# Kernel tuning notes

Measured on AMD Instinct MI355X. Metric: run time of the kernel, lower is better.

The kernel has to match this reference:

```python
import jax, jax.numpy as jnp
import numpy as np

TYPE_NUM = 4
CHILDS = [2, 2, 2, 2]
NODE_NUM = 8          # sum(CHILDS)
HEADS = 4
GROUP = 4
IN, MID, OUT = 256, 256, 256


def _mask():
    m = np.zeros((TYPE_NUM, NODE_NUM), np.float32)
    s = 0
    for i, c in enumerate(CHILDS):
        m[i, s:s + c] = 1.0
        s += c
    return jnp.asarray(m)


def _graph_feature(x, node_num):
    # x: [B, L, C] -> [B, M, node_num+1, C] with M = (L-1)//node_num
    B, L, C = x.shape
    node_x = x[:, 1:, :].reshape(B, -1, C * node_num)
    M = node_x.shape[1]
    src = x[:, :M, :]
    return jnp.concatenate([node_x, src], axis=2).reshape(B, M, node_num + 1, C)


def _conv1d(x, w, b, groups):
    # x: [N, C, T], w: [O, C//groups, K], stride == K, 'VALID' -> length-1 output
    y = jax.lax.conv_general_dilated(
        x, w, window_strides=(w.shape[-1],), padding='VALID',
        feature_group_count=groups, dimension_numbers=('NCH', 'OIH', 'NCH'))
    return y + b[None, :, None]


def _agg(feat, attn, mask):
    # feat: [B, M, node_num+1, C]; attn: [B, M, node_num, HEADS] (softmaxed)
    B, M, A, C = feat.shape
    n = A - 1
    nf = feat[:, :, :-1, :].reshape(B, M, n, HEADS, C // HEADS) * attn[..., None]
    nf = nf.reshape(B, M, n, C)
    agg = jnp.einsum('tn,bmnc->bmtc', mask, nf)  # masked group-sum (bmm with block mask)
    return agg, feat[:, :, -1, :]


def setup_inputs() -> dict:
    key = jax.random.key(0)
    ks = jax.random.split(key, 12)
    B, L = 4, 32777

    def lin(k, fi, fo):
        return jax.random.normal(k, (fi, fo), jnp.float32) / np.sqrt(fi).astype(np.float32)

    def convw(k, o, i, kk):
        return jax.random.normal(k, (o, i, kk), jnp.float32) / np.sqrt(i * kk).astype(np.float32)

    return {
        'input': jax.random.normal(ks[0], (B, L, IN), jnp.float32),
        'gt': jax.random.normal(ks[1], (B, 512, IN), jnp.float32),
        'w_att': lin(ks[2], IN, HEADS), 'b_att': jnp.zeros((HEADS,), jnp.float32),
        'w_gt1': lin(ks[3], IN, MID), 'b_gt1': jnp.zeros((MID,), jnp.float32),
        'w_gt2': lin(ks[4], MID, OUT), 'b_gt2': jnp.zeros((OUT,), jnp.float32),
        'w_agg1': convw(ks[5], MID, IN // GROUP, TYPE_NUM), 'b_agg1': jnp.zeros((MID,), jnp.float32),
        'w_src1': convw(ks[6], MID, IN // GROUP, 1), 'b_src1': jnp.zeros((MID,), jnp.float32),
        'w_agg2': convw(ks[7], OUT, MID // GROUP, TYPE_NUM), 'b_agg2': jnp.zeros((OUT,), jnp.float32),
        'w_src2': convw(ks[8], OUT, MID // GROUP, 1), 'b_src2': jnp.zeros((OUT,), jnp.float32),
    }


def reference(input, gt, w_att, b_att, w_gt1, b_gt1, w_gt2, b_gt2,
              w_agg1, b_agg1, w_src1, b_src1, w_agg2, b_agg2, w_src2, b_src2):
    mask = _mask()
    B = gt.shape[0]
    # gt branch (eval mode: dropout = identity)
    gt1 = jax.nn.relu(gt @ w_gt1 + b_gt1)   # [B, 512, MID]
    gt2 = jax.nn.relu(gt1 @ w_gt2 + b_gt2)  # [B, 512, OUT]

    # ---- layer 1 ----
    feat = _graph_feature(input, NODE_NUM)   # [B, M, 9, IN]
    M = feat.shape[1]
    ft = feat[:, :, -1:, :] + feat[:, :, :-1, :]          # source + each neighbor
    attn = jax.nn.softmax(ft @ w_att + b_att, axis=2)     # softmax over node dim
    node, src = _agg(feat, attn, mask)                    # [B,M,T,IN], [B,M,IN]
    BM = B * M
    node = jnp.transpose(node.reshape(BM, TYPE_NUM, IN), (0, 2, 1))  # [BM, IN, T]
    src = src.reshape(BM, IN, 1)
    node1 = jax.nn.relu(_conv1d(node, w_agg1, b_agg1, GROUP))[:, :, 0]  # [BM, MID]
    src1 = jax.nn.relu(_conv1d(src, w_src1, b_src1, GROUP))[:, :, 0]

    nf1 = node1.reshape(B, M, MID)[:, 0, :]
    d1 = gt1[:, 0, :] - nf1
    score1 = 1.0 - jnp.exp(-0.5 * jnp.sum(d1 * d1, axis=1))  # [B]

    out1 = (node1 + src1).reshape(B, M, MID)

    # ---- layer 2 (reuses attn truncated to M2) ----
    feat2 = _graph_feature(out1, NODE_NUM)  # [B, M2, 9, MID]
    M2 = feat2.shape[1]
    node2, src2 = _agg(feat2, attn[:, :M2], mask)
    BM2 = B * M2
    node2 = jnp.transpose(node2.reshape(BM2, TYPE_NUM, MID), (0, 2, 1))
    src2 = src2.reshape(BM2, MID, 1)
    node2c = jax.nn.relu(_conv1d(node2, w_agg2, b_agg2, GROUP))  # [BM2, OUT, 1]

    nf2 = node2c.reshape(B, M2, OUT)
    d2 = (gt2[:, :M2, :] - nf2).reshape(-1, OUT)
    score2 = 1.0 - jnp.exp(-0.5 * jnp.sum(d2 * d2, axis=1))  # [B*M2]

    src2c = jax.nn.relu(_conv1d(src2, w_src2, b_src2, GROUP))
    output = (node2c + src2c).reshape(-1, OUT)  # [B*M2, OUT]
    return output, score1, score2
```

## Files before the change

### kernel.cpp

```cpp
#include <hip/hip_runtime.h>

typedef unsigned short u16;
typedef unsigned int   u32;
typedef __attribute__((ext_vector_type(8))) short short8;
typedef __attribute__((ext_vector_type(4))) float f32x4;

#define BB  4
#define LL  32777
#define MM  4097
#define MMP 4112
#define MM2 512

__device__ __forceinline__ float b2f(u16 u) { return __uint_as_float(((u32)u) << 16); }
__device__ __forceinline__ u16 f2bf(float f) {
    u32 u = __float_as_uint(f);
    return (u16)((u + 0x7fffu + ((u >> 16) & 1u)) >> 16);
}
__device__ __forceinline__ u32 pk(float a, float b) {
    return (u32)f2bf(a) | ((u32)f2bf(b) << 16);
}
__device__ __forceinline__ float bflo(u32 u) { return __uint_as_float(u << 16); }
__device__ __forceinline__ float bfhi(u32 u) { return __uint_as_float(u & 0xffff0000u); }

__global__ __launch_bounds__(256) void prep_w(const float* __restrict__ wagg1,
                                              const float* __restrict__ wagg2,
                                              const float* __restrict__ wsrc1,
                                              const float* __restrict__ wsrc2,
                                              const float* __restrict__ watt,
                                              u16* __restrict__ wA1, u16* __restrict__ wA2,
                                              u16* __restrict__ wS1, u16* __restrict__ wS2,
                                              u16* __restrict__ wattB) {
    int idx = blockIdx.x * 256 + threadIdx.x;
    if (idx < 131072) {
        int which = idx >> 16;
        int e = idx & 65535;
        int j = e & 7, lane = (e >> 3) & 63, mt = (e >> 9) & 3, kc = (e >> 11) & 7, g = (e >> 14) & 3;
        int ol = mt * 16 + (lane & 15);
        int k = kc * 32 + (lane >> 4) * 8 + j;
        int t = k >> 6, ci = k & 63;
        const float* src = which ? wagg2 : wagg1;
        u16* dst = which ? wA2 : wA1;
        dst[e] = f2bf(src[(g * 64 + ol) * 256 + ci * 4 + t]);
    } else if (idx < 163840) {
        int e2 = idx - 131072;
        int which = e2 >> 14;
        int e = e2 & 16383;
        int j = e & 7, lane = (e >> 3) & 63, mt = (e >> 9) & 3, kc = (e >> 11) & 1, g = (e >> 12) & 3;
        int ol = mt * 16 + (lane & 15);
        int k = kc * 32 + (lane >> 4) * 8 + j;
        const float* src = which ? wsrc2 : wsrc1;
        u16* dst = which ? wS2 : wS1;
        dst[e] = f2bf(src[(g * 64 + ol) * 64 + k]);
    } else if (idx < 167936) {
        int e = idx - 163840;
        int j = e & 7, lane = (e >> 3) & 63, kc = e >> 9;
        int h = lane & 15, quad = lane >> 4;
        int k = kc * 32 + quad * 8 + j;
        wattB[e] = (h < 4) ? f2bf(watt[k * 4 + h]) : (u16)0;
    }
}

__global__ __launch_bounds__(256) void gemm2_fused_k(
    const float* __restrict__ gt, const float* __restrict__ W1, const float* __restrict__ b1,
    const float* __restrict__ W2, const float* __restrict__ b2,
    float* __restrict__ gt2, float* __restrict__ gt1m0) {
    __shared__ float sh[256][8];
    int tid = threadIdx.x;
    int row0 = blockIdx.x * 8;
    {
        int r = tid >> 5, j = tid & 31;
        const float4* a4 = (const float4*)(gt + (size_t)(row0 + r) * 256 + j * 8);
        float4 v0 = a4[0], v1 = a4[1];
        sh[j * 8 + 0][r] = v0.x; sh[j * 8 + 1][r] = v0.y;
        sh[j * 8 + 2][r] = v0.z; sh[j * 8 + 3][r] = v0.w;
        sh[j * 8 + 4][r] = v1.x; sh[j * 8 + 5][r] = v1.y;
        sh[j * 8 + 6][r] = v1.z; sh[j * 8 + 7][r] = v1.w;
    }
    __syncthreads();
    int o = tid;
    float acc[8];
    {
        float bo = b1[o];
        #pragma unroll
        for (int i = 0; i < 8; ++i) acc[i] = bo;
    }
    #pragma unroll 4
    for (int k = 0; k < 256; ++k) {
        float wv = W1[k * 256 + o];
        const float4* ap = (const float4*)&sh[k][0];
        float4 a0 = ap[0], a1 = ap[1];
        acc[0] = fmaf(a0.x, wv, acc[0]); acc[1] = fmaf(a0.y, wv, acc[1]);
        acc[2] = fmaf(a0.z, wv, acc[2]); acc[3] = fmaf(a0.w, wv, acc[3]);
        acc[4] = fmaf(a1.x, wv, acc[4]); acc[5] = fmaf(a1.y, wv, acc[5]);
        acc[6] = fmaf(a1.z, wv, acc[6]); acc[7] = fmaf(a1.w, wv, acc[7]);
    }
    #pragma unroll
    for (int i = 0; i < 8; ++i) acc[i] = fmaxf(acc[i], 0.f);
    if ((row0 & 511) == 0) gt1m0[(row0 >> 9) * 256 + o] = acc[0];
    __syncthreads();
    #pragma unroll
    for (int i = 0; i < 8; ++i) sh[o][i] = acc[i];
    __syncthreads();
    {
        float bo = b2[o];
        #pragma unroll
        for (int i = 0; i < 8; ++i) acc[i] = bo;
    }
    #pragma unroll 4
    for (int k = 0; k < 256; ++k) {
        float wv = W2[k * 256 + o];
        const float4* ap = (const float4*)&sh[k][0];
        float4 a0 = ap[0], a1 = ap[1];
        acc[0] = fmaf(a0.x, wv, acc[0]); acc[1] = fmaf(a0.y, wv, acc[1]);
        acc[2] = fmaf(a0.z, wv, acc[2]); acc[3] = fmaf(a0.w, wv, acc[3]);
        acc[4] = fmaf(a1.x, wv, acc[4]); acc[5] = fmaf(a1.y, wv, acc[5]);
        acc[6] = fmaf(a1.z, wv, acc[6]); acc[7] = fmaf(a1.w, wv, acc[7]);
    }
    #pragma unroll
    for (int i = 0; i < 8; ++i) gt2[(size_t)(row0 + i) * 256 + o] = fmaxf(acc[i], 0.f);
}

__global__ __launch_bounds__(256, 2) void l1fused_k(
    const float* __restrict__ x, const float* __restrict__ batt,
    const u16* __restrict__ wA1, const u16* __restrict__ wS1,
    const u16* __restrict__ wattB,
    const float* __restrict__ bagg1, const float* __restrict__ bsrc1,
    float* __restrict__ attnf, u16* __restrict__ out1, float* __restrict__ n1m0) {
    __shared__ u16   sh_node[128 * 256];
    __shared__ u16   sh_srcq[16 * 256];
    __shared__ float shR[1088];

    int tid = threadIdx.x;
    int lane = tid & 63, w = tid >> 6;
    int quad = lane >> 4;
    int b = blockIdx.y;
    int p0 = blockIdx.x * 16;

    {
        int cseg = lane & 15;
        int rsub = lane >> 4;
        const float* xb = x + (size_t)b * LL * 256;
        #pragma unroll
        for (int i = 0; i < 9; ++i) {
            int r = (w * 9 + i) * 4 + rsub;
            int grow, key; u16* dst;
            if (r < 128) {
                int pos = r >> 3, nn = r & 7;
                int gp = p0 + pos; int gpc = gp < MM ? gp : MM - 1;
                grow = 1 + 8 * gpc + nn;
                dst = sh_node + r * 256;
                key = ((r >> 3) ^ r) & 7;
            } else {
                int q = r - 128;
                int gp = p0 + q; int gpc = gp < MM ? gp : MM - 1;
                grow = gpc;
                dst = sh_srcq + q * 256;
                key = q & 7;
            }
            const float4* src4 = (const float4*)(xb + (size_t)grow * 256 + cseg * 16);
            float4 v0 = src4[0], v1 = src4[1], v2 = src4[2], v3 = src4[3];
            uint4 o0, o1;
            o0.x = pk(v0.x, v0.y); o0.y = pk(v0.z, v0.w);
            o0.z = pk(v1.x, v1.y); o0.w = pk(v1.z, v1.w);
            o1.x = pk(v2.x, v2.y); o1.y = pk(v2.z, v2.w);
            o1.z = pk(v3.x, v3.y); o1.w = pk(v3.z, v3.w);
            int cb0 = cseg * 2;
            *(uint4*)(dst + ((cb0 ^ key) * 8))       = o0;
            *(uint4*)(dst + (((cb0 + 1) ^ key) * 8)) = o1;
        }
    }
    __syncthreads();

    {
        short8 wB[8];
        #pragma unroll
        for (int kc = 0; kc < 8; ++kc) wB[kc] = *(const short8*)(wattB + kc * 512 + lane * 8);
        int m = lane & 15;
        int h = lane & 15;
        #pragma unroll
        for (int ti = 0; ti < 2; ++ti) {
            int mt = w * 2 + ti;
            int r = mt * 16 + m;
            int key = ((r >> 3) ^ r) & 7;
            const u16* rowp = sh_node + r * 256;
            f32x4 acc = (f32x4){0.f, 0.f, 0.f, 0.f};
            #pragma unroll
            for (int kc = 0; kc < 8; ++kc) {
                int cb = kc * 4 + quad;
                short8 aF = *(const short8*)(rowp + ((cb ^ key) * 8));
                acc = __builtin_amdgcn_mfma_f32_16x16x32_bf16(aF, wB[kc], acc, 0, 0, 0);
            }
            if (h < 4) {
                #pragma unroll
                for (int r2 = 0; r2 < 4; ++r2)
                    shR[(mt * 16 + quad * 4 + r2) * 4 + h] = acc[r2];
            }
        }
        if (w == 3) {
            int key = m & 7;
            const u16* rowp = sh_srcq + m * 256;
            f32x4 acc = (f32x4){0.f, 0.f, 0.f, 0.f};
            #pragma unroll
            for (int kc = 0; kc < 8; ++kc) {
                int cb = kc * 4 + quad;
                short8 aF = *(const short8*)(rowp + ((cb ^ key) * 8));
                acc = __builtin_amdgcn_mfma_f32_16x16x32_bf16(aF, wB[kc], acc, 0, 0, 0);
            }
            if (h < 4) {
                #pragma unroll
                for (int r2 = 0; r2 < 4; ++r2)
                    shR[512 + (quad * 4 + r2) * 4 + h] = acc[r2];
            }
        }
    }
    __syncthreads();

    if (tid < 64) {
        int q = tid >> 2, h = tid & 3;
        float base = shR[512 + q * 4 + h] + batt[h];
        float l[8], mx = -3.0e38f;
        #pragma unroll
        for (int n = 0; n < 8; ++n) { l[n] = shR[(q * 8 + n) * 4 + h] + base; mx = fmaxf(mx, l[n]); }
        float s = 0.f;
        #pragma unroll
        for (int n = 0; n < 8; ++n) { l[n] = __expf(l[n] - mx); s += l[n]; }
        float inv = 1.f / s;
        int gp = p0 + q;
        float* at = shR + 576;
        #pragma unroll
        for (int n = 0; n < 8; ++n) {
            float aa = l[n] * inv;
            at[(n * 4 + h) * 16 + q] = aa;
            if (gp < MM2) attnf[(((size_t)b * MM2 + gp) * 8 + n) * 4 + h] = aa;
        }
    }
    __syncthreads();

    int g = w;
    int col = lane & 15;
    float aT[8];
    {
        const float* at = shR + 576;
        #pragma unroll
        for (int nn = 0; nn < 8; ++nn) aT[nn] = at[(nn * 4 + g) * 16 + col];
    }
    f32x4 accn[4], accs[4];
    #pragma unroll
    for (int mt = 0; mt < 4; ++mt) { accn[mt] = (f32x4){0,0,0,0}; accs[mt] = (f32x4){0,0,0,0}; }

    #pragma unroll
    for (int kc = 0; kc < 8; ++kc) {
        int k0 = kc * 32 + quad * 8;
        int t = k0 >> 6, ci0 = k0 & 63;
        int cb = (g * 64 + ci0) >> 3;
        int r0 = col * 8 + 2 * t;
        int key0 = (col ^ (2 * t)) & 7, key1 = (col ^ (2 * t + 1)) & 7;
        short8 n0 = *(const short8*)(sh_node + r0 * 256 + ((cb ^ key0) * 8));
        short8 n1 = *(const short8*)(sh_node + (r0 + 1) * 256 + ((cb ^ key1) * 8));
        float a0 = aT[2 * t], a1 = aT[2 * t + 1];
        union { uint4 u; short8 s; } cv;
        #pragma unroll
        for (int e = 0; e < 4; ++e) {
            float lo = fmaf(a0, b2f((u16)n0[2 * e]),     a1 * b2f((u16)n1[2 * e]));
            float hi = fmaf(a0, b2f((u16)n0[2 * e + 1]), a1 * b2f((u16)n1[2 * e + 1]));
            ((u32*)&cv.u)[e] = pk(lo, hi);
        }
        short8 bB = cv.s;
        #pragma unroll
        for (int mt = 0; mt < 4; ++mt) {
            short8 aA = *(const short8*)(wA1 + (((g * 8 + kc) * 4 + mt) * 512 + lane * 8));
            accn[mt] = __builtin_amdgcn_mfma_f32_16x16x32_bf16(aA, bB, accn[mt], 0, 0, 0);
        }
    }
    #pragma unroll
    for (int kc = 0; kc < 2; ++kc) {
        int cb = (g * 64 + kc * 32 + quad * 8) >> 3;
        short8 bS = *(const short8*)(sh_srcq + col * 256 + ((cb ^ (col & 7)) * 8));
        #pragma unroll
        for (int mt = 0; mt < 4; ++mt) {
            short8 aS = *(const short8*)(wS1 + (((g * 2 + kc) * 4 + mt) * 512 + lane * 8));
            accs[mt] = __builtin_amdgcn_mfma_f32_16x16x32_bf16(aS, bS, accs[mt], 0, 0, 0);
        }
    }
    __syncthreads();

    u16* outt = sh_srcq;
    #pragma unroll
    for (int mt = 0; mt < 4; ++mt) {
        int ob = g * 64 + mt * 16 + quad * 4;
        float v[4], n1v[4];
        #pragma unroll
        for (int r = 0; r < 4; ++r) {
            int o = ob + r;
            float n1 = fmaxf(accn[mt][r] + bagg1[o], 0.f);
            float s1 = fmaxf(accs[mt][r] + bsrc1[o], 0.f);
            n1v[r] = n1;
            v[r] = n1 + s1;
        }
        u32* wp = (u32*)&outt[col * 256 + ob];
        wp[0] = pk(v[0], v[1]);
        wp[1] = pk(v[2], v[3]);
        if (blockIdx.x == 0 && col == 0) {
            #pragma unroll
            for (int r = 0; r < 4; ++r) n1m0[b * 256 + ob + r] = n1v[r];
        }
    }
    __syncthreads();
    for (int j = tid; j < 512; j += 256) {
        int pos = j >> 5, cc = (j & 31) * 8;
        if (p0 + pos < MM)
            *(uint4*)&out1[((size_t)b * MMP + p0 + pos) * 256 + cc] = *(const uint4*)&outt[pos * 256 + cc];
    }
}

__global__ __launch_bounds__(256) void score1_k(const float* __restrict__ gt1m0,
                                                const float* __restrict__ n1m0,
                                                float* __restrict__ score1p) {
    int b = blockIdx.x, tid = threadIdx.x;
    __shared__ float red[4];
    float d = gt1m0[b * 256 + tid] - n1m0[b * 256 + tid];
    float v = d * d;
    #pragma unroll
    for (int off = 32; off > 0; off >>= 1) v += __shfl_down(v, off, 64);
    if ((tid & 63) == 0) red[tid >> 6] = v;
    __syncthreads();
    if (tid == 0) score1p[b] = 1.f - __expf(-0.5f * (red[0] + red[1] + red[2] + red[3]));
}

__global__ __launch_bounds__(256) void l2conv_k(
    const u16* __restrict__ out1, const float* __restrict__ attnf,
    const float* __restrict__ gt2,
    const u16* __restrict__ wA2, const u16* __restrict__ wS2,
    const float* __restrict__ bagg2, const float* __restrict__ bsrc2,
    float* __restrict__ outp, float* __restrict__ score2p) {
    __shared__ char shraw[16 * 268 * 4 * 2];
    __shared__ float shred[128];

    int tid = threadIdx.x;
    int b = blockIdx.y;
    int p0 = blockIdx.x * 8;
    u16* aggl = (u16*)shraw;

    {
        int pos16 = tid >> 4, cc = tid & 15;
        int pos = pos16 < 8 ? pos16 : 7;
        int m = p0 + pos;
        int c0 = cc * 16;
        int h = c0 >> 6;
        const float* arow = attnf + ((size_t)b * MM2 + m) * 32;
        #pragma unroll
        for (int t = 0; t < 4; ++t) {
            float a0 = arow[(2 * t) * 4 + h];
            float a1 = arow[(2 * t + 1) * 4 + h];
            const uint4* r0 = (const uint4*)(out1 + ((size_t)b * MMP + 1 + 8 * m + 2 * t) * 256 + c0);
            const uint4* r1 = (const uint4*)(out1 + ((size_t)b * MMP + 2 + 8 * m + 2 * t) * 256 + c0);
            u32 w[8];
            #pragma unroll
            for (int v = 0; v < 2; ++v) {
                uint4 p = r0[v], q = r1[v];
                u32 pv[4] = {p.x, p.y, p.z, p.w};
                u32 qv[4] = {q.x, q.y, q.z, q.w};
                #pragma unroll
                for (int e = 0; e < 4; ++e) {
                    float lo = fmaf(bflo(pv[e]), a0, bflo(qv[e]) * a1);
                    float hi = fmaf(bfhi(pv[e]), a0, bfhi(qv[e]) * a1);
                    w[v * 4 + e] = pk(lo, hi);
                }
            }
            u32* dst = (u32*)&aggl[pos16 * 1024 + h * 256 + t * 64 + (c0 & 63)];
            ((uint4*)dst)[0] = make_uint4(w[0], w[1], w[2], w[3]);
            ((uint4*)dst)[1] = make_uint4(w[4], w[5], w[6], w[7]);
        }
    }
    __syncthreads();

    int lane = tid & 63, g = tid >> 6;
    int col = lane & 15, quad = lane >> 4;
    f32x4 accn[4], accs[4];
    #pragma unroll
    for (int mt = 0; mt < 4; ++mt) { accn[mt] = (f32x4){0,0,0,0}; accs[mt] = (f32x4){0,0,0,0}; }

    #pragma unroll
    for (int kc = 0; kc < 8; ++kc) {
        short8 bB = *(const short8*)&aggl[col * 1024 + g * 256 + kc * 32 + quad * 8];
        #pragma unroll
        for (int mt = 0; mt < 4; ++mt) {
            short8 aA = *(const short8*)(wA2 + (((g * 8 + kc) * 4 + mt) * 512 + lane * 8));
            accn[mt] = __builtin_amdgcn_mfma_f32_16x16x32_bf16(aA, bB, accn[mt], 0, 0, 0);
        }
    }
    {
        int pcol = col < 8 ? col : 7;
        #pragma unroll
        for (int kc = 0; kc < 2; ++kc) {
            short8 bS = *(const short8*)(out1 + ((size_t)b * MMP + p0 + pcol) * 256 + g * 64 + kc * 32 + quad * 8);
            #pragma unroll
            for (int mt = 0; mt < 4; ++mt) {
                short8 aS = *(const short8*)(wS2 + (((g * 2 + kc) * 4 + mt) * 512 + lane * 8));
                accs[mt] = __builtin_amdgcn_mfma_f32_16x16x32_bf16(aS, bS, accs[mt], 0, 0, 0);
            }
        }
    }
    __syncthreads();

    float* outt = (float*)shraw;
    float* n2t  = outt + 16 * 268;
    #pragma unroll
    for (int mt = 0; mt < 4; ++mt) {
        #pragma unroll
        for (int r = 0; r < 4; ++r) {
            int o = g * 64 + mt * 16 + quad * 4 + r;
            float n2 = fmaxf(accn[mt][r] + bagg2[o], 0.f);
            float s2 = fmaxf(accs[mt][r] + bsrc2[o], 0.f);
            outt[col * 268 + o] = n2 + s2;
            n2t[col * 268 + o] = n2;
        }
    }
    __syncthreads();

    for (int j = tid; j < 512; j += 256) {
        int pos = j >> 6, cc = (j & 63) * 4;
        *(float4*)&outp[((size_t)b * MM2 + p0 + pos) * 256 + cc] = *(const float4*)&outt[pos * 268 + cc];
    }
    if (tid < 128) {
        int pos = tid >> 4, kk = tid & 15;
        const float* grow = gt2 + ((size_t)b * MM2 + p0 + pos) * 256 + kk * 16;
        const float* nrow = n2t + pos * 268 + kk * 16;
        float s = 0.f;
        #pragma unroll
        for (int c = 0; c < 16; ++c) { float d = grow[c] - nrow[c]; s = fmaf(d, d, s); }
        shred[pos * 16 + kk] = s;
    }
    __syncthreads();
    if (tid < 8) {
        float s = 0.f;
        #pragma unroll
        for (int kk = 0; kk < 16; ++kk) s += shred[tid * 16 + kk];
        score2p[(size_t)b * MM2 + p0 + tid] = 1.f - __expf(-0.5f * s);
    }
}

extern "C" void kernel_launch(void* const* d_in, const int* in_sizes, int n_in,
                              void* d_out, int out_size, void* d_ws, size_t ws_size,
                              hipStream_t stream) {
    const float* x     = (const float*)d_in[0];
    const float* gt    = (const float*)d_in[1];
    const float* watt  = (const float*)d_in[2];
    const float* batt  = (const float*)d_in[3];
    const float* wgt1  = (const float*)d_in[4];
    const float* bgt1  = (const float*)d_in[5];
    const float* wgt2  = (const float*)d_in[6];
    const float* bgt2  = (const float*)d_in[7];
    const float* wagg1 = (const float*)d_in[8];
    const float* bagg1 = (const float*)d_in[9];
    const float* wsrc1 = (const float*)d_in[10];
    const float* bsrc1 = (const float*)d_in[11];
    const float* wagg2 = (const float*)d_in[12];
    const float* bagg2 = (const float*)d_in[13];
    const float* wsrc2 = (const float*)d_in[14];
    const float* bsrc2 = (const float*)d_in[15];

    char* ws = (char*)d_ws;
    float* ws_gt2  = (float*)(ws + 0);
    float* attnf   = (float*)(ws + 2097152);
    float* n1m0    = (float*)(ws + 2359296);
    float* gt1m0   = (float*)(ws + 2363392);
    u16*   wA1     = (u16*)(ws + 2367488);
    u16*   wS1     = (u16*)(ws + 2498560);
    u16*   wA2     = (u16*)(ws + 2531328);
    u16*   wS2     = (u16*)(ws + 2662400);
    u16*   wattB   = (u16*)(ws + 2695168);
    u16*   out1    = (u16*)(ws + 2703360);

    float* outp    = (float*)d_out;
    float* score1p = outp + 524288;
    float* score2p = outp + 524292;

    prep_w<<<dim3(656), dim3(256), 0, stream>>>(wagg1, wagg2, wsrc1, wsrc2, watt,
                                                wA1, wA2, wS1, wS2, wattB);
    gemm2_fused_k<<<dim3(256), dim3(256), 0, stream>>>(gt, wgt1, bgt1, wgt2, bgt2, ws_gt2, gt1m0);
    l1fused_k<<<dim3(257, 4), dim3(256), 0, stream>>>(x, batt, wA1, wS1, wattB, bagg1, bsrc1,
                                                      attnf, out1, n1m0);
    score1_k<<<dim3(4), dim3(256), 0, stream>>>(gt1m0, n1m0, score1p);
    l2conv_k<<<dim3(64, 4), dim3(256), 0, stream>>>(out1, attnf, ws_gt2, wA2, wS2, bagg2, bsrc2,
                                                    outp, score2p);
}
```

Baseline: 307.1 us.

## Halve l1fused tile to raise occupancy and merge small kernels into neighbors

The layer-1 fused kernel now handles 8 positions per block instead of 16. That halves its shared memory, raises the launch-bounds occupancy target from 2 to 4, and doubles the grid. The weight-prep and gt GEMM kernels are merged into one launch, and the score1 reduction becomes an extra block column of the layer-2 kernel, cutting the launch count from five to three. The price is half-filled MFMA tiles in the source path (only 8 of 16 columns are useful) and more redundant weight loads per block.

```diff
diff --git a/kernel.cpp b/kernel.cpp
--- a/kernel.cpp
+++ b/kernel.cpp
@@ -22,51 +22,49 @@
 __device__ __forceinline__ float bflo(u32 u) { return __uint_as_float(u << 16); }
 __device__ __forceinline__ float bfhi(u32 u) { return __uint_as_float(u & 0xffff0000u); }
 
-__global__ __launch_bounds__(256) void prep_w(const float* __restrict__ wagg1,
-                                              const float* __restrict__ wagg2,
-                                              const float* __restrict__ wsrc1,
-                                              const float* __restrict__ wsrc2,
-                                              const float* __restrict__ watt,
-                                              u16* __restrict__ wA1, u16* __restrict__ wA2,
-                                              u16* __restrict__ wS1, u16* __restrict__ wS2,
-                                              u16* __restrict__ wattB) {
-    int idx = blockIdx.x * 256 + threadIdx.x;
-    if (idx < 131072) {
-        int which = idx >> 16;
-        int e = idx & 65535;
-        int j = e & 7, lane = (e >> 3) & 63, mt = (e >> 9) & 3, kc = (e >> 11) & 7, g = (e >> 14) & 3;
-        int ol = mt * 16 + (lane & 15);
-        int k = kc * 32 + (lane >> 4) * 8 + j;
-        int t = k >> 6, ci = k & 63;
-        const float* src = which ? wagg2 : wagg1;
-        u16* dst = which ? wA2 : wA1;
-        dst[e] = f2bf(src[(g * 64 + ol) * 256 + ci * 4 + t]);
-    } else if (idx < 163840) {
-        int e2 = idx - 131072;
-        int which = e2 >> 14;
-        int e = e2 & 16383;
-        int j = e & 7, lane = (e >> 3) & 63, mt = (e >> 9) & 3, kc = (e >> 11) & 1, g = (e >> 12) & 3;
-        int ol = mt * 16 + (lane & 15);
-        int k = kc * 32 + (lane >> 4) * 8 + j;
-        const float* src = which ? wsrc2 : wsrc1;
-        u16* dst = which ? wS2 : wS1;
-        dst[e] = f2bf(src[(g * 64 + ol) * 64 + k]);
-    } else if (idx < 167936) {
-        int e = idx - 163840;
-        int j = e & 7, lane = (e >> 3) & 63, kc = e >> 9;
-        int h = lane & 15, quad = lane >> 4;
-        int k = kc * 32 + quad * 8 + j;
-        wattB[e] = (h < 4) ? f2bf(watt[k * 4 + h]) : (u16)0;
-    }
-}
-
-__global__ __launch_bounds__(256) void gemm2_fused_k(
+__global__ __launch_bounds__(256) void setup_k(
+    const float* __restrict__ wagg1, const float* __restrict__ wagg2,
+    const float* __restrict__ wsrc1, const float* __restrict__ wsrc2,
+    const float* __restrict__ watt,
+    u16* __restrict__ wA1, u16* __restrict__ wA2,
+    u16* __restrict__ wS1, u16* __restrict__ wS2, u16* __restrict__ wattB,
     const float* __restrict__ gt, const float* __restrict__ W1, const float* __restrict__ b1,
     const float* __restrict__ W2, const float* __restrict__ b2,
     float* __restrict__ gt2, float* __restrict__ gt1m0) {
     __shared__ float sh[256][8];
     int tid = threadIdx.x;
-    int row0 = blockIdx.x * 8;
+    if (blockIdx.x < 656) {
+        int idx = blockIdx.x * 256 + tid;
+        if (idx < 131072) {
+            int which = idx >> 16;
+            int e = idx & 65535;
+            int j = e & 7, lane = (e >> 3) & 63, mt = (e >> 9) & 3, kc = (e >> 11) & 7, g = (e >> 14) & 3;
+            int ol = mt * 16 + (lane & 15);
+            int k = kc * 32 + (lane >> 4) * 8 + j;
+            int t = k >> 6, ci = k & 63;
+            const float* src = which ? wagg2 : wagg1;
+            u16* dst = which ? wA2 : wA1;
+            dst[e] = f2bf(src[(g * 64 + ol) * 256 + ci * 4 + t]);
+        } else if (idx < 163840) {
+            int e2 = idx - 131072;
+            int which = e2 >> 14;
+            int e = e2 & 16383;
+            int j = e & 7, lane = (e >> 3) & 63, mt = (e >> 9) & 3, kc = (e >> 11) & 1, g = (e >> 12) & 3;
+            int ol = mt * 16 + (lane & 15);
+            int k = kc * 32 + (lane >> 4) * 8 + j;
+            const float* src = which ? wsrc2 : wsrc1;
+            u16* dst = which ? wS2 : wS1;
+            dst[e] = f2bf(src[(g * 64 + ol) * 64 + k]);
+        } else {
+            int e = idx - 163840;
+            int j = e & 7, lane = (e >> 3) & 63, kc = e >> 9;
+            int h = lane & 15, quad = lane >> 4;
+            int k = kc * 32 + quad * 8 + j;
+            wattB[e] = (h < 4) ? f2bf(watt[k * 4 + h]) : (u16)0;
+        }
+        return;
+    }
+    int row0 = (blockIdx.x - 656) * 8;
     {
         int r = tid >> 5, j = tid & 31;
         const float4* a4 = (const float4*)(gt + (size_t)(row0 + r) * 256 + j * 8);
@@ -120,53 +118,54 @@
     for (int i = 0; i < 8; ++i) gt2[(size_t)(row0 + i) * 256 + o] = fmaxf(acc[i], 0.f);
 }
 
-__global__ __launch_bounds__(256, 2) void l1fused_k(
+__global__ __launch_bounds__(256, 4) void l1fused_k(
     const float* __restrict__ x, const float* __restrict__ batt,
     const u16* __restrict__ wA1, const u16* __restrict__ wS1,
     const u16* __restrict__ wattB,
     const float* __restrict__ bagg1, const float* __restrict__ bsrc1,
     float* __restrict__ attnf, u16* __restrict__ out1, float* __restrict__ n1m0) {
-    __shared__ u16   sh_node[128 * 256];
-    __shared__ u16   sh_srcq[16 * 256];
-    __shared__ float shR[1088];
+    __shared__ u16   sh_node[64 * 256];
+    __shared__ u16   sh_srcq[8 * 256];
+    __shared__ float shR[576];
 
     int tid = threadIdx.x;
     int lane = tid & 63, w = tid >> 6;
     int quad = lane >> 4;
     int b = blockIdx.y;
-    int p0 = blockIdx.x * 16;
-
-    {
-        int cseg = lane & 15;
-        int rsub = lane >> 4;
+    int p0 = blockIdx.x * 8;
+
+    {
+        int rslot = tid >> 4, cseg = tid & 15;
         const float* xb = x + (size_t)b * LL * 256;
         #pragma unroll
-        for (int i = 0; i < 9; ++i) {
-            int r = (w * 9 + i) * 4 + rsub;
-            int grow, key; u16* dst;
-            if (r < 128) {
-                int pos = r >> 3, nn = r & 7;
-                int gp = p0 + pos; int gpc = gp < MM ? gp : MM - 1;
-                grow = 1 + 8 * gpc + nn;
-                dst = sh_node + r * 256;
-                key = ((r >> 3) ^ r) & 7;
-            } else {
-                int q = r - 128;
-                int gp = p0 + q; int gpc = gp < MM ? gp : MM - 1;
-                grow = gpc;
-                dst = sh_srcq + q * 256;
-                key = q & 7;
-            }
-            const float4* src4 = (const float4*)(xb + (size_t)grow * 256 + cseg * 16);
-            float4 v0 = src4[0], v1 = src4[1], v2 = src4[2], v3 = src4[3];
-            uint4 o0, o1;
-            o0.x = pk(v0.x, v0.y); o0.y = pk(v0.z, v0.w);
-            o0.z = pk(v1.x, v1.y); o0.w = pk(v1.z, v1.w);
-            o1.x = pk(v2.x, v2.y); o1.y = pk(v2.z, v2.w);
-            o1.z = pk(v3.x, v3.y); o1.w = pk(v3.z, v3.w);
-            int cb0 = cseg * 2;
-            *(uint4*)(dst + ((cb0 ^ key) * 8))       = o0;
-            *(uint4*)(dst + (((cb0 + 1) ^ key) * 8)) = o1;
+        for (int pass = 0; pass < 5; ++pass) {
+            int r = pass * 16 + rslot;
+            if (r < 72) {
+                int grow, key; u16* dst;
+                if (r < 64) {
+                    int pos = r >> 3, nn = r & 7;
+                    int gp = p0 + pos; int gpc = gp < MM ? gp : MM - 1;
+                    grow = 1 + 8 * gpc + nn;
+                    dst = sh_node + r * 256;
+                    key = (pos ^ nn) & 7;
+                } else {
+                    int q = r - 64;
+                    int gp = p0 + q; int gpc = gp < MM ? gp : MM - 1;
+                    grow = gpc;
+                    dst = sh_srcq + q * 256;
+                    key = q & 7;
+                }
+                const float4* src4 = (const float4*)(xb + (size_t)grow * 256 + cseg * 16);
+                float4 v0 = src4[0], v1 = src4[1], v2 = src4[2], v3 = src4[3];
+                uint4 o0, o1;
+                o0.x = pk(v0.x, v0.y); o0.y = pk(v0.z, v0.w);
+                o0.z = pk(v1.x, v1.y); o0.w = pk(v1.z, v1.w);
+                o1.x = pk(v2.x, v2.y); o1.y = pk(v2.z, v2.w);
+                o1.z = pk(v3.x, v3.y); o1.w = pk(v3.z, v3.w);
+                int cb0 = cseg * 2;
+                *(uint4*)(dst + ((cb0 ^ key) * 8))       = o0;
+                *(uint4*)(dst + (((cb0 + 1) ^ key) * 8)) = o1;
+            }
         }
     }
     __syncthreads();
@@ -177,11 +176,9 @@
         for (int kc = 0; kc < 8; ++kc) wB[kc] = *(const short8*)(wattB + kc * 512 + lane * 8);
         int m = lane & 15;
         int h = lane & 15;
-        #pragma unroll
-        for (int ti = 0; ti < 2; ++ti) {
-            int mt = w * 2 + ti;
-            int r = mt * 16 + m;
-            int key = ((r >> 3) ^ r) & 7;
+        {
+            int r = w * 16 + m;
+            int key = ((r >> 3) ^ (r & 7)) & 7;
             const u16* rowp = sh_node + r * 256;
             f32x4 acc = (f32x4){0.f, 0.f, 0.f, 0.f};
             #pragma unroll
@@ -193,12 +190,13 @@
             if (h < 4) {
                 #pragma unroll
                 for (int r2 = 0; r2 < 4; ++r2)
-                    shR[(mt * 16 + quad * 4 + r2) * 4 + h] = acc[r2];
+                    shR[(w * 16 + quad * 4 + r2) * 4 + h] = acc[r2];
             }
         }
         if (w == 3) {
-            int key = m & 7;
-            const u16* rowp = sh_srcq + m * 256;
+            int ms = m < 8 ? m : 7;
+            int key = ms & 7;
+            const u16* rowp = sh_srcq + ms * 256;
             f32x4 acc = (f32x4){0.f, 0.f, 0.f, 0.f};
             #pragma unroll
             for (int kc = 0; kc < 8; ++kc) {
@@ -208,16 +206,18 @@
             }
             if (h < 4) {
                 #pragma unroll
-                for (int r2 = 0; r2 < 4; ++r2)
-                    shR[512 + (quad * 4 + r2) * 4 + h] = acc[r2];
-            }
-        }
-    }
-    __syncthreads();
-
-    if (tid < 64) {
+                for (int r2 = 0; r2 < 4; ++r2) {
+                    int rr = quad * 4 + r2;
+                    if (rr < 8) shR[256 + rr * 4 + h] = acc[r2];
+                }
+            }
+        }
+    }
+    __syncthreads();
+
+    if (tid < 32) {
         int q = tid >> 2, h = tid & 3;
-        float base = shR[512 + q * 4 + h] + batt[h];
+        float base = shR[256 + q * 4 + h] + batt[h];
         float l[8], mx = -3.0e38f;
         #pragma unroll
         for (int n = 0; n < 8; ++n) { l[n] = shR[(q * 8 + n) * 4 + h] + base; mx = fmaxf(mx, l[n]); }
@@ -226,11 +226,11 @@
         for (int n = 0; n < 8; ++n) { l[n] = __expf(l[n] - mx); s += l[n]; }
         float inv = 1.f / s;
         int gp = p0 + q;
-        float* at = shR + 576;
+        float* at = shR + 320;
         #pragma unroll
         for (int n = 0; n < 8; ++n) {
             float aa = l[n] * inv;
-            at[(n * 4 + h) * 16 + q] = aa;
+            at[(n * 4 + h) * 8 + q] = aa;
             if (gp < MM2) attnf[(((size_t)b * MM2 + gp) * 8 + n) * 4 + h] = aa;
         }
     }
@@ -238,11 +238,12 @@
 
     int g = w;
     int col = lane & 15;
+    int pos = col & 7;
     float aT[8];
     {
-        const float* at = shR + 576;
-        #pragma unroll
-        for (int nn = 0; nn < 8; ++nn) aT[nn] = at[(nn * 4 + g) * 16 + col];
+        const float* at = shR + 320;
+        #pragma unroll
+        for (int nn = 0; nn < 8; ++nn) aT[nn] = at[(nn * 4 + g) * 8 + pos];
     }
     f32x4 accn[4], accs[4];
     #pragma unroll
@@ -253,8 +254,8 @@
         int k0 = kc * 32 + quad * 8;
         int t = k0 >> 6, ci0 = k0 & 63;
         int cb = (g * 64 + ci0) >> 3;
-        int r0 = col * 8 + 2 * t;
-        int key0 = (col ^ (2 * t)) & 7, key1 = (col ^ (2 * t + 1)) & 7;
+        int r0 = pos * 8 + 2 * t;
+        int key0 = (pos ^ (2 * t)) & 7, key1 = (pos ^ (2 * t + 1)) & 7;
         short8 n0 = *(const short8*)(sh_node + r0 * 256 + ((cb ^ key0) * 8));
         short8 n1 = *(const short8*)(sh_node + (r0 + 1) * 256 + ((cb ^ key1) * 8));
         float a0 = aT[2 * t], a1 = aT[2 * t + 1];
@@ -275,7 +276,7 @@
     #pragma unroll
     for (int kc = 0; kc < 2; ++kc) {
         int cb = (g * 64 + kc * 32 + quad * 8) >> 3;
-        short8 bS = *(const short8*)(sh_srcq + col * 256 + ((cb ^ (col & 7)) * 8));
+        short8 bS = *(const short8*)(sh_srcq + pos * 256 + ((cb ^ pos) * 8));
         #pragma unroll
         for (int mt = 0; mt < 4; ++mt) {
             short8 aS = *(const short8*)(wS1 + (((g * 2 + kc) * 4 + mt) * 512 + lane * 8));
@@ -297,34 +298,22 @@
             n1v[r] = n1;
             v[r] = n1 + s1;
         }
-        u32* wp = (u32*)&outt[col * 256 + ob];
-        wp[0] = pk(v[0], v[1]);
-        wp[1] = pk(v[2], v[3]);
+        if (col < 8) {
+            u32* wp = (u32*)&outt[col * 256 + ob];
+            wp[0] = pk(v[0], v[1]);
+            wp[1] = pk(v[2], v[3]);
+        }
         if (blockIdx.x == 0 && col == 0) {
             #pragma unroll
             for (int r = 0; r < 4; ++r) n1m0[b * 256 + ob + r] = n1v[r];
         }
     }
     __syncthreads();
-    for (int j = tid; j < 512; j += 256) {
-        int pos = j >> 5, cc = (j & 31) * 8;
-        if (p0 + pos < MM)
-            *(uint4*)&out1[((size_t)b * MMP + p0 + pos) * 256 + cc] = *(const uint4*)&outt[pos * 256 + cc];
-    }
-}
-
-__global__ __launch_bounds__(256) void score1_k(const float* __restrict__ gt1m0,
-                                                const float* __restrict__ n1m0,
-                                                float* __restrict__ score1p) {
-    int b = blockIdx.x, tid = threadIdx.x;
-    __shared__ float red[4];
-    float d = gt1m0[b * 256 + tid] - n1m0[b * 256 + tid];
-    float v = d * d;
-    #pragma unroll
-    for (int off = 32; off > 0; off >>= 1) v += __shfl_down(v, off, 64);
-    if ((tid & 63) == 0) red[tid >> 6] = v;
-    __syncthreads();
-    if (tid == 0) score1p[b] = 1.f - __expf(-0.5f * (red[0] + red[1] + red[2] + red[3]));
+    {
+        int posw = tid >> 5, cc = (tid & 31) * 8;
+        if (p0 + posw < MM)
+            *(uint4*)&out1[((size_t)b * MMP + p0 + posw) * 256 + cc] = *(const uint4*)&outt[posw * 256 + cc];
+    }
 }
 
 __global__ __launch_bounds__(256) void l2conv_k(
@@ -332,12 +321,25 @@
     const float* __restrict__ gt2,
     const u16* __restrict__ wA2, const u16* __restrict__ wS2,
     const float* __restrict__ bagg2, const float* __restrict__ bsrc2,
-    float* __restrict__ outp, float* __restrict__ score2p) {
+    const float* __restrict__ gt1m0, const float* __restrict__ n1m0,
+    float* __restrict__ outp, float* __restrict__ score2p, float* __restrict__ score1p) {
     __shared__ char shraw[16 * 268 * 4 * 2];
     __shared__ float shred[128];
 
     int tid = threadIdx.x;
     int b = blockIdx.y;
+
+    if (blockIdx.x == 64) {
+        float d = gt1m0[b * 256 + tid] - n1m0[b * 256 + tid];
+        float v = d * d;
+        #pragma unroll
+        for (int off = 32; off > 0; off >>= 1) v += __shfl_down(v, off, 64);
+        if ((tid & 63) == 0) shred[tid >> 6] = v;
+        __syncthreads();
+        if (tid == 0) score1p[b] = 1.f - __expf(-0.5f * (shred[0] + shred[1] + shred[2] + shred[3]));
+        return;
+    }
+
     int p0 = blockIdx.x * 8;
     u16* aggl = (u16*)shraw;
 
@@ -476,12 +478,11 @@
     float* score1p = outp + 524288;
     float* score2p = outp + 524292;
 
-    prep_w<<<dim3(656), dim3(256), 0, stream>>>(wagg1, wagg2, wsrc1, wsrc2, watt,
-                                                wA1, wA2, wS1, wS2, wattB);
-    gemm2_fused_k<<<dim3(256), dim3(256), 0, stream>>>(gt, wgt1, bgt1, wgt2, bgt2, ws_gt2, gt1m0);
-    l1fused_k<<<dim3(257, 4), dim3(256), 0, stream>>>(x, batt, wA1, wS1, wattB, bagg1, bsrc1,
+    setup_k<<<dim3(912), dim3(256), 0, stream>>>(wagg1, wagg2, wsrc1, wsrc2, watt,
+                                                 wA1, wA2, wS1, wS2, wattB,
+                                                 gt, wgt1, bgt1, wgt2, bgt2, ws_gt2, gt1m0);
+    l1fused_k<<<dim3(513, 4), dim3(256), 0, stream>>>(x, batt, wA1, wS1, wattB, bagg1, bsrc1,
                                                       attnf, out1, n1m0);
-    score1_k<<<dim3(4), dim3(256), 0, stream>>>(gt1m0, n1m0, score1p);
-    l2conv_k<<<dim3(64, 4), dim3(256), 0, stream>>>(out1, attnf, ws_gt2, wA2, wS2, bagg2, bsrc2,
-                                                    outp, score2p);
-}
+    l2conv_k<<<dim3(65, 4), dim3(256), 0, stream>>>(out1, attnf, ws_gt2, wA2, wS2, bagg2, bsrc2,
+                                                    gt1m0, n1m0, outp, score2p, score1p);
+}
```

New measurement: 300.5 us. -2.1%, faster.
